# Kernel optimization log

Measured on AMD Instinct MI355X. Metric: run time of the kernel, lower is better.

## Reference

```python
import jax, jax.numpy as jnp
import numpy as np

# Static network configuration (from the cfg json in the original module)
BPL = [1, 1536, 1536, 1536, 1536]            # buckets per layer; layer 0 must be 1 (original code indexes inflows[0] only)
L = len(BPL)
NSPIG = [BPL[l + 1] if l < L - 1 else 1 for l in range(L)]  # spigots per bucket in each layer
MAX_B = max(BPL)
MAX_S = max(NSPIG)
G = 9.81
T = 4                                         # number of update_network timesteps


def _spigot_mask():
    # mask[l, b, s] = 1 if bucket b and spigot s exist in layer l (matches the zero-padding in initialize_theta_values)
    m = np.zeros((L, MAX_B, MAX_S), np.float32)
    for l in range(L):
        m[l, :BPL[l], :NSPIG[l]] = 1.0
    return jnp.asarray(m)


def _solve_layer(H0b, sp_h_l, sp_a_l, th_l):
    """Vectorized solve_single_bucket across all buckets of one layer.
    H0b: [B] head after adding inflow. sp_h_l/sp_a_l/th_l: [B, S].
    Sequential over spigots: H_effective = H0b - cumsum(flows)/2.
    Returns (H_new [B], s_q [B, S])."""
    def step(cum, x):
        hh, aa, tt = x                         # each [B]
        h = jnp.maximum(0.0, H0b - 0.5 * cum - hh)
        # safe sqrt (same forward value; avoids nan grad at h == 0)
        v = tt * jnp.sqrt(2.0 * G * jnp.where(h > 0, h, 1.0))
        flow = jnp.where(h > 0, v * aa, 0.0)
        return cum + flow, flow

    xs = (sp_h_l.T, sp_a_l.T, th_l.T)          # [S, B]
    Q, flows = jax.lax.scan(step, jnp.zeros_like(H0b), xs)
    return H0b - Q, flows.T                    # H = (H + inflow) - sum(s_q)


def setup_inputs() -> dict:
    key = jax.random.key(0)
    k1, k2, k3, k4 = jax.random.split(key, 4)
    theta = jax.random.uniform(k1, (L, MAX_B, MAX_S), jnp.float32)   # padded theta table
    sp_h = jax.random.uniform(k2, (L, MAX_B, MAX_S), jnp.float32)    # spigot heights
    sp_a = jax.random.uniform(k3, (L, MAX_B, MAX_S), jnp.float32)    # spigot areas
    H_init = jnp.ones((L, MAX_B), jnp.float32)                        # initial_head_in_buckets = 1.0
    precip = jax.random.uniform(k4, (T,), jnp.float32)                # precip per update step
    return {"theta": theta, "sp_h": sp_h, "sp_a": sp_a, "H_init": H_init, "precip": precip}


def reference(theta, sp_h, sp_a, H_init, precip):
    mask = _spigot_mask()
    theta_m = theta * mask                     # zero theta on padded buckets/spigots -> zero flows there

    def step_t(H_all, p):
        ppl = p / L                            # precip_inflow_per_layer
        H_new = []
        sq_prev = None
        for l in range(L):
            if l == 0:
                inflow = jnp.zeros((MAX_B,), H_all.dtype).at[0].set(ppl)
            else:
                # inflow[j] = sum over upstream buckets of s_q[i, j] + ppl / n_buckets
                inflow = sq_prev.sum(axis=0) + ppl / BPL[l]
            Hn, sq = _solve_layer(H_all[l] + inflow, sp_h[l], sp_a[l], theta_m[l])
            H_new.append(Hn)
            sq_prev = sq
        # network_outflow = sum of last layer s_q
        return jnp.stack(H_new), sq_prev.sum()

    _, outflows = jax.lax.scan(step_t, H_init, precip)
    return outflows                            # [T] network outflow per update step
```

## Files before the change

### kernel.cpp

```cpp
#include <hip/hip_runtime.h>

#define NB 1536
#define NS 1536
#define TSTEPS 4
#define KC  4.4294469180704688f
#define HKC 2.2147234590352344f

#define OFF_KHT 0ull
#define OFF_KH0 (OFF_KHT + 3ull * NS * NB * 8)
#define OFF_KH4 (OFF_KH0 + (unsigned long long)NS * 8)
#define OFF_H   (OFF_KH4 + (unsigned long long)NB * 8)
#define OFF_FB0 (OFF_H + 5ull * NB * 4)
#define OFF_PART (OFF_FB0 + 2ull * NS * 4)

static __device__ __forceinline__ float asqrt(float x) { return __builtin_amdgcn_sqrtf(x); }

#define SSTEP2(HK, HY, SLOC)                \
  {                                         \
    float e_ = fmaxf(R - (HY), 0.0f);       \
    float q_ = asqrt(e_);                   \
    R = fmaf(-(HK), q_, R);                 \
    red[SLOC][lane] = (HK)*q_;              \
  }

#define LOADB(P0,P1,P2,P3,P4,P5,P6,P7, sp)                        \
  { const float2* q_ = kh + (size_t)(sp) * NB;                    \
    P0 = q_[0];            P1 = q_[(size_t)NB];                   \
    P2 = q_[2*(size_t)NB]; P3 = q_[3*(size_t)NB];                 \
    P4 = q_[4*(size_t)NB]; P5 = q_[5*(size_t)NB];                 \
    P6 = q_[6*(size_t)NB]; P7 = q_[7*(size_t)NB]; }

#define CONS8(P0,P1,P2,P3,P4,P5,P6,P7, SL)                        \
  { SSTEP2(P0.x,P0.y,(SL)+0) SSTEP2(P1.x,P1.y,(SL)+1)             \
    SSTEP2(P2.x,P2.y,(SL)+2) SSTEP2(P3.x,P3.y,(SL)+3)             \
    SSTEP2(P4.x,P4.y,(SL)+4) SSTEP2(P5.x,P5.y,(SL)+5)             \
    SSTEP2(P6.x,P6.y,(SL)+6) SSTEP2(P7.x,P7.y,(SL)+7) }

__global__ __launch_bounds__(256) void prep_small_k(const float* __restrict__ th,
                                                    const float* __restrict__ hh,
                                                    const float* __restrict__ aa,
                                                    float2* __restrict__ kh0,
                                                    float2* __restrict__ kh4) {
  int i = blockIdx.x * 256 + threadIdx.x;
  if (i >= NS) return;
  kh0[i] = make_float2(th[i] * aa[i] * HKC, hh[i]);
  size_t i4 = ((size_t)4 * NB + i) * NS;
  kh4[i] = make_float2(th[i4] * aa[i4] * KC, hh[i4]);
}

__global__ __launch_bounds__(256) void transpose_k(const float* __restrict__ th,
                                                   const float* __restrict__ hh,
                                                   const float* __restrict__ aa,
                                                   float2* __restrict__ khT) {
  __shared__ float2 tile[64][65];
  int l = blockIdx.z + 1;
  int b0 = blockIdx.x * 64, s0 = blockIdx.y * 64;
  int lane = threadIdx.x & 63, ty = threadIdx.x >> 6;
  size_t base = (size_t)l * NB * NS;
#pragma unroll
  for (int r = 0; r < 64; r += 4) {
    int b = b0 + r + ty;
    size_t idx = base + (size_t)b * NS + s0 + lane;
    tile[r + ty][lane] = make_float2(th[idx] * aa[idx] * HKC, hh[idx]);
  }
  __syncthreads();
#pragma unroll
  for (int r = 0; r < 64; r += 4) {
    int s = s0 + r + ty;
    khT[((size_t)blockIdx.z * NS + s) * NB + b0 + lane] = tile[lane][r + ty];
  }
}

__global__ void init_k(const float* __restrict__ Hinit, float* __restrict__ H,
                       float* __restrict__ out) {
  int i = blockIdx.x * 256 + threadIdx.x;
  if (i < 5 * NB) H[i] = Hinit[i];
  if (i < TSTEPS) out[i] = 0.0f;
}

static __device__ void scan0(const float2* __restrict__ kh0, float* __restrict__ fbrow,
                             float* __restrict__ H0, float P) {
  float R = P;
  const float4* p = (const float4*)kh0;
  float4 c0 = p[0], c1 = p[1], c2 = p[2], c3 = p[3];
#define SSTEP0(HK, HY, S)                                          \
  { float e_ = fmaxf(R - (HY), 0.0f); float q_ = asqrt(e_);        \
    R = fmaf(-(HK), q_, R); fbrow[S] = (HK)*q_; }
#pragma unroll 1
  for (int s = 0; s < NS; s += 8) {
    int np_ = (s + 8 < NS) ? (s + 8) >> 1 : 0;
    float4 n0 = p[np_], n1 = p[np_ + 1], n2 = p[np_ + 2], n3 = p[np_ + 3];
    SSTEP0(c0.x, c0.y, s + 0) SSTEP0(c0.z, c0.w, s + 1)
    SSTEP0(c1.x, c1.y, s + 2) SSTEP0(c1.z, c1.w, s + 3)
    SSTEP0(c2.x, c2.y, s + 4) SSTEP0(c2.z, c2.w, s + 5)
    SSTEP0(c3.x, c3.y, s + 6) SSTEP0(c3.z, c3.w, s + 7)
    c0 = n0; c1 = n1; c2 = n2; c3 = n3;
  }
  *H0 = 2.0f * R - P;
}

__global__ __launch_bounds__(64) void stage_k(
    const float2* __restrict__ khT, const float2* __restrict__ kh0,
    const float2* __restrict__ kh4, float* __restrict__ H,
    float* __restrict__ fb0, float* __restrict__ part,
    const float* __restrict__ precip, float* __restrict__ out, int d) {
  __shared__ float red[32][64];
  int blk = blockIdx.x;
  int lane = threadIdx.x;

  if (blk == 96) {
    int t = d;
    if (t >= TSTEPS || lane != 0) return;
    float P = H[0] + precip[t] * 0.2f;
    scan0(kh0, fb0 + (size_t)(t & 1) * NS, H, P);
    return;
  }
  int track = blk / 24, b = blk % 24;
  int l = track + 1;
  int t = d - l;
  if (t < 0 || t >= TSTEPS) return;
  int par = t & 1;
  float ppl = precip[t] * 0.2f;
  int j = b * 64 + lane;

  if (l == 4) {
    const float* pr = part + ((size_t)(2 * 2 + par) * 24) * NS + j;
    float s_ = 0.f;
#pragma unroll
    for (int i = 0; i < 24; ++i) s_ += pr[(size_t)i * NS];
    float P = H[4 * NB + j] + 2.0f * s_ + ppl * (1.0f / NB);
    float2 kh = kh4[j];
    float e = fmaxf(P - kh.y, 0.0f);
    float fl = kh.x * asqrt(e);
    H[4 * NB + j] = P - fl;
    for (int o = 32; o; o >>= 1) fl += __shfl_xor(fl, o);
    if (lane == 0) atomicAdd(out + t, fl);
    return;
  }

  float inf;
  if (l == 1) {
    inf = 2.0f * fb0[(size_t)par * NS + j];
  } else {
    const float* pr = part + ((size_t)((l - 2) * 2 + par) * 24) * NS + j;
    float s_ = 0.f;
#pragma unroll
    for (int i = 0; i < 24; ++i) s_ += pr[(size_t)i * NS];
    inf = 2.0f * s_;
  }
  float P = H[l * NB + j] + inf + ppl * (1.0f / NB);
  float R = P;
  const float2* kh = khT + (size_t)(l - 1) * NS * NB + j;
  float* part_row = part + ((size_t)((l - 1) * 2 + par) * 24 + b) * NS;

  float2 A0,A1,A2,A3,A4,A5,A6,A7, B0,B1,B2,B3,B4,B5,B6,B7;
  float2 C0,C1,C2,C3,C4,C5,C6,C7, D0,D1,D2,D3,D4,D5,D6,D7;
  LOADB(A0,A1,A2,A3,A4,A5,A6,A7, 0)
  LOADB(B0,B1,B2,B3,B4,B5,B6,B7, 8)
  LOADB(C0,C1,C2,C3,C4,C5,C6,C7, 16)
  LOADB(D0,D1,D2,D3,D4,D5,D6,D7, 24)
  int rs = lane >> 1, rh = (lane & 1) * 32;
#pragma unroll 1
  for (int s = 0; s < NS; s += 32) {
    int s1 = (s + 32 < NS) ? s + 32 : 0;
    CONS8(A0,A1,A2,A3,A4,A5,A6,A7, 0)
    LOADB(A0,A1,A2,A3,A4,A5,A6,A7, s1)
    CONS8(B0,B1,B2,B3,B4,B5,B6,B7, 8)
    LOADB(B0,B1,B2,B3,B4,B5,B6,B7, s1 + 8)
    CONS8(C0,C1,C2,C3,C4,C5,C6,C7, 16)
    LOADB(C0,C1,C2,C3,C4,C5,C6,C7, s1 + 16)
    CONS8(D0,D1,D2,D3,D4,D5,D6,D7, 24)
    LOADB(D0,D1,D2,D3,D4,D5,D6,D7, s1 + 24)
    {
      const float* rowp = &red[rs][rh];
      float acc = 0.f;
#pragma unroll
      for (int c = 0; c < 32; ++c) acc += rowp[(c + lane) & 31];
      acc += __shfl_xor(acc, 1);
      if (!(lane & 1)) part_row[s + rs] = acc;
    }
  }
  H[l * NB + j] = 2.0f * R - P;
}

extern "C" void kernel_launch(void* const* d_in, const int* in_sizes, int n_in,
                              void* d_out, int out_size, void* d_ws,
                              size_t ws_size, hipStream_t stream) {
  const float* theta = (const float*)d_in[0];
  const float* sp_h = (const float*)d_in[1];
  const float* sp_a = (const float*)d_in[2];
  const float* Hinit = (const float*)d_in[3];
  const float* precip = (const float*)d_in[4];
  float* out = (float*)d_out;

  char* ws = (char*)d_ws;
  float2* khT = (float2*)(ws + OFF_KHT);
  float2* kh0 = (float2*)(ws + OFF_KH0);
  float2* kh4 = (float2*)(ws + OFF_KH4);
  float* H = (float*)(ws + OFF_H);
  float* fb0 = (float*)(ws + OFF_FB0);
  float* part = (float*)(ws + OFF_PART);

  hipLaunchKernelGGL(prep_small_k, dim3(6), dim3(256), 0, stream, theta, sp_h,
                     sp_a, kh0, kh4);
  hipLaunchKernelGGL(transpose_k, dim3(24, 24, 3), dim3(256), 0, stream, theta,
                     sp_h, sp_a, khT);
  hipLaunchKernelGGL(init_k, dim3(30), dim3(256), 0, stream, Hinit, H, out);

  for (int d = 0; d < TSTEPS + 4; ++d) {
    hipLaunchKernelGGL(stage_k, dim3(97), dim3(64), 0, stream, khT, kh0, kh4, H,
                       fb0, part, precip, out, d);
  }
}
```

Measured before the change: 552.9 us.

## Overlap layer-0 scan with transpose, deepen prefetch, stage kh0 in LDS

Result: faster. 467.2 us (-15.5%).

```diff
diff --git a/kernel.cpp b/kernel.cpp
--- a/kernel.cpp
+++ b/kernel.cpp
@@ -15,44 +15,95 @@
 
 static __device__ __forceinline__ float asqrt(float x) { return __builtin_amdgcn_sqrtf(x); }
 
-#define SSTEP2(HK, HY, SLOC)                \
+#define SS0(HK, HY, F)                      \
   {                                         \
     float e_ = fmaxf(R - (HY), 0.0f);       \
     float q_ = asqrt(e_);                   \
     R = fmaf(-(HK), q_, R);                 \
-    red[SLOC][lane] = (HK)*q_;              \
-  }
-
-#define LOADB(P0,P1,P2,P3,P4,P5,P6,P7, sp)                        \
+    F = (HK)*q_;                            \
+  }
+
+#define SST(HK, HY, SL)                     \
+  {                                         \
+    float e_ = fmaxf(R - (HY), 0.0f);       \
+    float q_ = asqrt(e_);                   \
+    R = fmaf(-(HK), q_, R);                 \
+    red[SL][lane] = (HK)*q_;                \
+  }
+
+#define LB(P0,P1,P2,P3,P4,P5,P6,P7, sp)                           \
   { const float2* q_ = kh + (size_t)(sp) * NB;                    \
     P0 = q_[0];            P1 = q_[(size_t)NB];                   \
     P2 = q_[2*(size_t)NB]; P3 = q_[3*(size_t)NB];                 \
     P4 = q_[4*(size_t)NB]; P5 = q_[5*(size_t)NB];                 \
     P6 = q_[6*(size_t)NB]; P7 = q_[7*(size_t)NB]; }
 
-#define CONS8(P0,P1,P2,P3,P4,P5,P6,P7, SL)                        \
-  { SSTEP2(P0.x,P0.y,(SL)+0) SSTEP2(P1.x,P1.y,(SL)+1)             \
-    SSTEP2(P2.x,P2.y,(SL)+2) SSTEP2(P3.x,P3.y,(SL)+3)             \
-    SSTEP2(P4.x,P4.y,(SL)+4) SSTEP2(P5.x,P5.y,(SL)+5)             \
-    SSTEP2(P6.x,P6.y,(SL)+6) SSTEP2(P7.x,P7.y,(SL)+7) }
-
-__global__ __launch_bounds__(256) void prep_small_k(const float* __restrict__ th,
-                                                    const float* __restrict__ hh,
-                                                    const float* __restrict__ aa,
-                                                    float2* __restrict__ kh0,
-                                                    float2* __restrict__ kh4) {
+#define CB(P0,P1,P2,P3,P4,P5,P6,P7, SL)                           \
+  { SST(P0.x,P0.y,(SL)+0) SST(P1.x,P1.y,(SL)+1)                   \
+    SST(P2.x,P2.y,(SL)+2) SST(P3.x,P3.y,(SL)+3)                   \
+    SST(P4.x,P4.y,(SL)+4) SST(P5.x,P5.y,(SL)+5)                   \
+    SST(P6.x,P6.y,(SL)+6) SST(P7.x,P7.y,(SL)+7) }
+
+static __device__ void scan0_lds(const float4* __restrict__ k0, float* __restrict__ fbrow,
+                                 float* __restrict__ H0, float P) {
+  float R = P;
+  float4 c0 = k0[0], c1 = k0[1], c2 = k0[2], c3 = k0[3];
+  float4 n0 = k0[4], n1 = k0[5], n2 = k0[6], n3 = k0[7];
+#pragma unroll 1
+  for (int g = 0; g < NS / 8; ++g) {
+    int mi = (g + 2 < NS / 8) ? 4 * g + 8 : 0;
+    float4 m0 = k0[mi], m1 = k0[mi + 1], m2 = k0[mi + 2], m3 = k0[mi + 3];
+    float f0, f1, f2, f3, f4, f5, f6, f7;
+    SS0(c0.x, c0.y, f0) SS0(c0.z, c0.w, f1)
+    SS0(c1.x, c1.y, f2) SS0(c1.z, c1.w, f3)
+    SS0(c2.x, c2.y, f4) SS0(c2.z, c2.w, f5)
+    SS0(c3.x, c3.y, f6) SS0(c3.z, c3.w, f7)
+    ((float4*)fbrow)[2 * g]     = make_float4(f0, f1, f2, f3);
+    ((float4*)fbrow)[2 * g + 1] = make_float4(f4, f5, f6, f7);
+    c0 = n0; c1 = n1; c2 = n2; c3 = n3;
+    n0 = m0; n1 = m1; n2 = m2; n3 = m3;
+  }
+  *H0 = 2.0f * R - P;
+}
+
+__global__ __launch_bounds__(256) void prep_k(const float* __restrict__ th,
+                                              const float* __restrict__ hh,
+                                              const float* __restrict__ aa,
+                                              const float* __restrict__ Hinit,
+                                              float2* __restrict__ kh0,
+                                              float2* __restrict__ kh4,
+                                              float* __restrict__ H,
+                                              float* __restrict__ out) {
   int i = blockIdx.x * 256 + threadIdx.x;
-  if (i >= NS) return;
-  kh0[i] = make_float2(th[i] * aa[i] * HKC, hh[i]);
-  size_t i4 = ((size_t)4 * NB + i) * NS;
-  kh4[i] = make_float2(th[i4] * aa[i4] * KC, hh[i4]);
+  if (i < NS) {
+    kh0[i] = make_float2(th[i] * aa[i] * HKC, hh[i]);
+    size_t i4 = ((size_t)4 * NB + i) * NS;
+    kh4[i] = make_float2(th[i4] * aa[i4] * KC, hh[i4]);
+  }
+  if (i < 5 * NB && i != 0) H[i] = Hinit[i];
+  if (i < TSTEPS) out[i] = 0.0f;
 }
 
 __global__ __launch_bounds__(256) void transpose_k(const float* __restrict__ th,
                                                    const float* __restrict__ hh,
                                                    const float* __restrict__ aa,
-                                                   float2* __restrict__ khT) {
+                                                   float2* __restrict__ khT,
+                                                   const float2* __restrict__ kh0,
+                                                   const float* __restrict__ Hinit,
+                                                   const float* __restrict__ precip,
+                                                   float* __restrict__ H,
+                                                   float* __restrict__ fb0) {
   __shared__ float2 tile[64][65];
+  __shared__ float4 k0lds[NS / 2];
+  if (blockIdx.z == 3) {
+    if (blockIdx.x || blockIdx.y) return;
+    int lane = threadIdx.x;
+    for (int i = lane; i < NS / 2; i += 256) k0lds[i] = ((const float4*)kh0)[i];
+    __syncthreads();
+    if (lane) return;
+    scan0_lds(k0lds, fb0 , H, Hinit[0] + precip[0] * 0.2f);
+    return;
+  }
   int l = blockIdx.z + 1;
   int b0 = blockIdx.x * 64, s0 = blockIdx.y * 64;
   int lane = threadIdx.x & 63, ty = threadIdx.x >> 6;
@@ -69,34 +120,6 @@
     int s = s0 + r + ty;
     khT[((size_t)blockIdx.z * NS + s) * NB + b0 + lane] = tile[lane][r + ty];
   }
-}
-
-__global__ void init_k(const float* __restrict__ Hinit, float* __restrict__ H,
-                       float* __restrict__ out) {
-  int i = blockIdx.x * 256 + threadIdx.x;
-  if (i < 5 * NB) H[i] = Hinit[i];
-  if (i < TSTEPS) out[i] = 0.0f;
-}
-
-static __device__ void scan0(const float2* __restrict__ kh0, float* __restrict__ fbrow,
-                             float* __restrict__ H0, float P) {
-  float R = P;
-  const float4* p = (const float4*)kh0;
-  float4 c0 = p[0], c1 = p[1], c2 = p[2], c3 = p[3];
-#define SSTEP0(HK, HY, S)                                          \
-  { float e_ = fmaxf(R - (HY), 0.0f); float q_ = asqrt(e_);        \
-    R = fmaf(-(HK), q_, R); fbrow[S] = (HK)*q_; }
-#pragma unroll 1
-  for (int s = 0; s < NS; s += 8) {
-    int np_ = (s + 8 < NS) ? (s + 8) >> 1 : 0;
-    float4 n0 = p[np_], n1 = p[np_ + 1], n2 = p[np_ + 2], n3 = p[np_ + 3];
-    SSTEP0(c0.x, c0.y, s + 0) SSTEP0(c0.z, c0.w, s + 1)
-    SSTEP0(c1.x, c1.y, s + 2) SSTEP0(c1.z, c1.w, s + 3)
-    SSTEP0(c2.x, c2.y, s + 4) SSTEP0(c2.z, c2.w, s + 5)
-    SSTEP0(c3.x, c3.y, s + 6) SSTEP0(c3.z, c3.w, s + 7)
-    c0 = n0; c1 = n1; c2 = n2; c3 = n3;
-  }
-  *H0 = 2.0f * R - P;
 }
 
 __global__ __launch_bounds__(64) void stage_k(
@@ -104,15 +127,18 @@
     const float2* __restrict__ kh4, float* __restrict__ H,
     float* __restrict__ fb0, float* __restrict__ part,
     const float* __restrict__ precip, float* __restrict__ out, int d) {
-  __shared__ float red[32][64];
+  __shared__ float red[64][64];
+  __shared__ float4 k0lds[NS / 2];
   int blk = blockIdx.x;
   int lane = threadIdx.x;
 
   if (blk == 96) {
     int t = d;
-    if (t >= TSTEPS || lane != 0) return;
-    float P = H[0] + precip[t] * 0.2f;
-    scan0(kh0, fb0 + (size_t)(t & 1) * NS, H, P);
+    if (t >= TSTEPS) return;
+    for (int i = lane; i < NS / 2; i += 64) k0lds[i] = ((const float4*)kh0)[i];
+    __syncthreads();
+    if (lane) return;
+    scan0_lds(k0lds, fb0 + (size_t)(t & 1) * NS, H, H[0] + precip[t] * 0.2f);
     return;
   }
   int track = blk / 24, b = blk % 24;
@@ -155,29 +181,37 @@
 
   float2 A0,A1,A2,A3,A4,A5,A6,A7, B0,B1,B2,B3,B4,B5,B6,B7;
   float2 C0,C1,C2,C3,C4,C5,C6,C7, D0,D1,D2,D3,D4,D5,D6,D7;
-  LOADB(A0,A1,A2,A3,A4,A5,A6,A7, 0)
-  LOADB(B0,B1,B2,B3,B4,B5,B6,B7, 8)
-  LOADB(C0,C1,C2,C3,C4,C5,C6,C7, 16)
-  LOADB(D0,D1,D2,D3,D4,D5,D6,D7, 24)
-  int rs = lane >> 1, rh = (lane & 1) * 32;
+  float2 E0,E1,E2,E3,E4,E5,E6,E7, F0,F1,F2,F3,F4,F5,F6,F7;
+  float2 G0,G1,G2,G3,G4,G5,G6,G7, X0,X1,X2,X3,X4,X5,X6,X7;
+  LB(A0,A1,A2,A3,A4,A5,A6,A7, 0)
+  LB(B0,B1,B2,B3,B4,B5,B6,B7, 8)
+  LB(C0,C1,C2,C3,C4,C5,C6,C7, 16)
+  LB(D0,D1,D2,D3,D4,D5,D6,D7, 24)
+  LB(E0,E1,E2,E3,E4,E5,E6,E7, 32)
+  LB(F0,F1,F2,F3,F4,F5,F6,F7, 40)
+  LB(G0,G1,G2,G3,G4,G5,G6,G7, 48)
+  LB(X0,X1,X2,X3,X4,X5,X6,X7, 56)
 #pragma unroll 1
-  for (int s = 0; s < NS; s += 32) {
-    int s1 = (s + 32 < NS) ? s + 32 : 0;
-    CONS8(A0,A1,A2,A3,A4,A5,A6,A7, 0)
-    LOADB(A0,A1,A2,A3,A4,A5,A6,A7, s1)
-    CONS8(B0,B1,B2,B3,B4,B5,B6,B7, 8)
-    LOADB(B0,B1,B2,B3,B4,B5,B6,B7, s1 + 8)
-    CONS8(C0,C1,C2,C3,C4,C5,C6,C7, 16)
-    LOADB(C0,C1,C2,C3,C4,C5,C6,C7, s1 + 16)
-    CONS8(D0,D1,D2,D3,D4,D5,D6,D7, 24)
-    LOADB(D0,D1,D2,D3,D4,D5,D6,D7, s1 + 24)
+  for (int s = 0; s < NS; s += 64) {
+    int sA = (s + 64 < NS) ? s + 64 : 0;
+    int sE = (s + 96 < NS) ? s + 96 : 0;
+    CB(A0,A1,A2,A3,A4,A5,A6,A7, 0)   LB(A0,A1,A2,A3,A4,A5,A6,A7, sA)
+    CB(B0,B1,B2,B3,B4,B5,B6,B7, 8)   LB(B0,B1,B2,B3,B4,B5,B6,B7, sA + 8)
+    CB(C0,C1,C2,C3,C4,C5,C6,C7, 16)  LB(C0,C1,C2,C3,C4,C5,C6,C7, sA + 16)
+    CB(D0,D1,D2,D3,D4,D5,D6,D7, 24)  LB(D0,D1,D2,D3,D4,D5,D6,D7, sA + 24)
+    CB(E0,E1,E2,E3,E4,E5,E6,E7, 32)  LB(E0,E1,E2,E3,E4,E5,E6,E7, sE)
+    CB(F0,F1,F2,F3,F4,F5,F6,F7, 40)  LB(F0,F1,F2,F3,F4,F5,F6,F7, sE + 8)
+    CB(G0,G1,G2,G3,G4,G5,G6,G7, 48)  LB(G0,G1,G2,G3,G4,G5,G6,G7, sE + 16)
+    CB(X0,X1,X2,X3,X4,X5,X6,X7, 56)  LB(X0,X1,X2,X3,X4,X5,X6,X7, sE + 24)
     {
-      const float* rowp = &red[rs][rh];
-      float acc = 0.f;
-#pragma unroll
-      for (int c = 0; c < 32; ++c) acc += rowp[(c + lane) & 31];
-      acc += __shfl_xor(acc, 1);
-      if (!(lane & 1)) part_row[s + rs] = acc;
+      const float4* rowq = (const float4*)&red[lane][0];
+      float a0 = 0.f, a1 = 0.f, a2 = 0.f, a3 = 0.f;
+#pragma unroll
+      for (int c = 0; c < 16; ++c) {
+        float4 v = rowq[(c + lane) & 15];
+        a0 += v.x; a1 += v.y; a2 += v.z; a3 += v.w;
+      }
+      part_row[s + lane] = (a0 + a1) + (a2 + a3);
     }
   }
   H[l * NB + j] = 2.0f * R - P;
@@ -201,13 +235,11 @@
   float* fb0 = (float*)(ws + OFF_FB0);
   float* part = (float*)(ws + OFF_PART);
 
-  hipLaunchKernelGGL(prep_small_k, dim3(6), dim3(256), 0, stream, theta, sp_h,
-                     sp_a, kh0, kh4);
-  hipLaunchKernelGGL(transpose_k, dim3(24, 24, 3), dim3(256), 0, stream, theta,
-                     sp_h, sp_a, khT);
-  hipLaunchKernelGGL(init_k, dim3(30), dim3(256), 0, stream, Hinit, H, out);
-
-  for (int d = 0; d < TSTEPS + 4; ++d) {
+  hipLaunchKernelGGL(prep_k, dim3(30), dim3(256), 0, stream, theta, sp_h, sp_a,
+                     Hinit, kh0, kh4, H, out);
+  hipLaunchKernelGGL(transpose_k, dim3(24, 24, 4), dim3(256), 0, stream, theta,
+                     sp_h, sp_a, khT, kh0, Hinit, precip, H, fb0);
+  for (int d = 1; d < TSTEPS + 4; ++d) {
     hipLaunchKernelGGL(stage_k, dim3(97), dim3(64), 0, stream, khT, kh0, kh4, H,
                        fb0, part, precip, out, d);
   }
```
